# Optimization experiments

Measured on AMD Instinct MI355X. Metric: run time of the kernel, lower is better.

Reference implementation:

```python
import jax, jax.numpy as jnp
import numpy as np

B, SQ, SK, D, H, DFF = 4, 1024, 1024, 1024, 16, 4096
DEPTH = D // H
EPS = 1e-6


def setup_inputs() -> dict:
    key = jax.random.key(0)
    ks = jax.random.split(key, 32)
    s = 0.02
    inp = {
        "x": jax.random.normal(ks[0], (B, SQ, D), jnp.float32),
        "enc_output": jax.random.normal(ks[1], (B, SK, D), jnp.float32),
        # causal look-ahead mask: 1 where attention is disallowed
        "look_ahead_mask": (1.0 - jnp.tril(jnp.ones((SQ, SQ), jnp.float32)))[None, None],
        "padding_mask": jnp.zeros((B, 1, 1, SK), jnp.float32),
    }
    names = ["wq1", "wk1", "wv1", "wo1", "wq2", "wk2", "wv2", "wo2"]
    for i, n in enumerate(names):
        inp[n] = jax.random.normal(ks[2 + i], (D, D), jnp.float32) * s
        inp["b" + n[1:]] = jnp.zeros((D,), jnp.float32)
    inp["w_ffn1"] = jax.random.normal(ks[12], (D, DFF), jnp.float32) * s
    inp["b_ffn1"] = jnp.zeros((DFF,), jnp.float32)
    inp["w_ffn2"] = jax.random.normal(ks[13], (DFF, D), jnp.float32) * s
    inp["b_ffn2"] = jnp.zeros((D,), jnp.float32)
    for i in (1, 2, 3):
        inp[f"gamma{i}"] = jnp.ones((D,), jnp.float32)
        inp[f"beta{i}"] = jnp.zeros((D,), jnp.float32)
    return inp


def _layernorm(x, gamma, beta):
    mu = jnp.mean(x, axis=-1, keepdims=True)
    var = jnp.var(x, axis=-1, keepdims=True)
    return (x - mu) * jax.lax.rsqrt(var + EPS) * gamma + beta


def _split_heads(x):
    b, s, _ = x.shape
    return x.reshape(b, s, H, DEPTH).transpose(0, 2, 1, 3)  # (B,H,S,depth)


def _mha(v_in, k_in, q_in, mask, wq, bq, wk, bk, wv, bv, wo, bo):
    q = _split_heads(q_in @ wq + bq)
    k = _split_heads(k_in @ wk + bk)
    v = _split_heads(v_in @ wv + bv)
    logits = jnp.einsum("bhqd,bhkd->bhqk", q, k) / jnp.sqrt(jnp.float32(DEPTH))
    if mask is not None:
        logits = logits + mask * -1e9
    attn = jax.nn.softmax(logits, axis=-1)
    out = jnp.einsum("bhqk,bhkd->bhqd", attn, v)
    out = out.transpose(0, 2, 1, 3).reshape(q_in.shape[0], -1, D)
    return out @ wo + bo, attn


def reference(x, enc_output, look_ahead_mask, padding_mask,
              wq1, bq1, wk1, bk1, wv1, bv1, wo1, bo1,
              wq2, bq2, wk2, bk2, wv2, bv2, wo2, bo2,
              w_ffn1, b_ffn1, w_ffn2, b_ffn2,
              gamma1, beta1, gamma2, beta2, gamma3, beta3):
    attn1, aw1 = _mha(x, x, x, look_ahead_mask,
                      wq1, bq1, wk1, bk1, wv1, bv1, wo1, bo1)
    out1 = _layernorm(attn1 + x, gamma1, beta1)
    attn2, aw2 = _mha(enc_output, enc_output, out1, padding_mask,
                      wq2, bq2, wk2, bk2, wv2, bv2, wo2, bo2)
    out2 = _layernorm(attn2 + out1, gamma2, beta2)
    ffn = jax.nn.relu(out2 @ w_ffn1 + b_ffn1) @ w_ffn2 + b_ffn2
    out3 = _layernorm(ffn + out2, gamma3, beta3)
    return out3, aw1, aw2
```

## Files before the change

kernel.cpp:

```cpp
#include <hip/hip_runtime.h>

#define NB 4
#define SEQ 1024
#define DM 1024
#define NH 16
#define DEP 64
#define DFFN 4096

typedef __attribute__((ext_vector_type(8))) short short8;
typedef __attribute__((ext_vector_type(4))) float f32x4;
typedef __attribute__((ext_vector_type(4))) unsigned short us4;

__device__ __forceinline__ unsigned short f2bf(float f) {
    union { float f; unsigned int u; } v; v.f = f;
    unsigned int u = v.u;
    return (unsigned short)((u + 0x7FFFu + ((u >> 16) & 1u)) >> 16);
}

__device__ __forceinline__ void gload16(const void* g, void* l) {
    __builtin_amdgcn_global_load_lds((const __attribute__((address_space(1))) unsigned int*)g,
                                     (__attribute__((address_space(3))) unsigned int*)l, 16, 0, 0);
}

__global__ __launch_bounds__(256) void cast2_kernel(const float* __restrict__ a,
                                                    const float* __restrict__ b,
                                                    unsigned short* __restrict__ oa,
                                                    unsigned short* __restrict__ ob, int n4) {
    int i = blockIdx.x * 256 + threadIdx.x;
    const float* in = blockIdx.y ? b : a;
    unsigned short* out = blockIdx.y ? ob : oa;
    if (i < n4) {
        float4 f = ((const float4*)in)[i];
        us4 u;
        u[0] = f2bf(f.x); u[1] = f2bf(f.y); u[2] = f2bf(f.z); u[3] = f2bf(f.w);
        ((us4*)out)[i] = u;
    }
}

struct P10 { const float* p[10]; };
__global__ __launch_bounds__(256) void castTall_kernel(P10 s,
                                                       unsigned short* __restrict__ wsq,
                                                       unsigned short* __restrict__ wf1t,
                                                       unsigned short* __restrict__ wf2t) {
    __shared__ float tile[64][65];
    const int tid = blockIdx.x, t = threadIdx.x;
    const float* in; unsigned short* out; int R, C, r0, c0;
    if (tid < 2048) {
        int wi = tid >> 8, t2 = tid & 255;
        in = s.p[wi]; out = wsq + (size_t)wi * DM * DM; R = DM; C = DM;
        r0 = (t2 >> 4) * 64; c0 = (t2 & 15) * 64;
    } else if (tid < 3072) {
        int t2 = tid - 2048;
        in = s.p[8]; out = wf1t; R = DM; C = DFFN;
        r0 = (t2 >> 6) * 64; c0 = (t2 & 63) * 64;
    } else {
        int t2 = tid - 3072;
        in = s.p[9]; out = wf2t; R = DFFN; C = DM;
        r0 = (t2 >> 4) * 64; c0 = (t2 & 15) * 64;
    }
#pragma unroll
    for (int p = 0; p < 4; ++p) {
        int r = p * 16 + (t >> 4), c = (t & 15) * 4;
        float4 f = *(const float4*)(in + (size_t)(r0 + r) * C + c0 + c);
        tile[r][c] = f.x; tile[r][c + 1] = f.y; tile[r][c + 2] = f.z; tile[r][c + 3] = f.w;
    }
    __syncthreads();
#pragma unroll
    for (int p = 0; p < 4; ++p) {
        int n = p * 16 + (t >> 4), k = (t & 15) * 4;
        us4 u;
#pragma unroll
        for (int j = 0; j < 4; ++j) u[j] = f2bf(tile[k + j][n]);
        *(us4*)(out + (size_t)(c0 + n) * R + r0 + k) = u;
    }
}

__global__ __launch_bounds__(256) void biaspack_kernel(const float* __restrict__ bq1,
                                                       const float* __restrict__ bk1,
                                                       const float* __restrict__ bv1,
                                                       const float* __restrict__ bk2,
                                                       const float* __restrict__ bv2,
                                                       float* __restrict__ bqkv1,
                                                       float* __restrict__ bkv2) {
    int i = blockIdx.x * 256 + threadIdx.x;
    if (i < 1024) bqkv1[i] = bq1[i];
    else if (i < 2048) bqkv1[i] = bk1[i - 1024];
    else if (i < 3072) bqkv1[i] = bv1[i - 2048];
    else if (i < 4096) bkv2[i - 3072] = bk2[i - 3072];
    else if (i < 5120) bkv2[i - 3072] = bv2[i - 4096];
}

template <int BM, int BN, int BK, int KSPLIT, int RELU, int WB, int WF, int WVT>
__global__ __launch_bounds__(256) void gemm_kernel(const unsigned short* __restrict__ A,
                                                   const unsigned short* __restrict__ Wt,
                                                   const float* __restrict__ bias,
                                                   unsigned short* __restrict__ Cb,
                                                   float* __restrict__ Cf,
                                                   float* __restrict__ Cf2,
                                                   unsigned short* __restrict__ Vt,
                                                   int vstart,
                                                   int M, int N, int K) {
    constexpr int AM = BM / 32;
    constexpr int KS = BK / 32;
    constexpr int LPR = BK / 8;
    constexpr int RPI = 64 / LPR;
    constexpr int AR = (BM / 4) / RPI;
    constexpr int BR = (BN / 4) / RPI;
    __shared__ unsigned short As[BM * BK];
    __shared__ unsigned short Bs[BN * BK];
    const int t = threadIdx.x;
    const int lane = t & 63, w = t >> 6;
    const int m0 = blockIdx.y * BM, n0 = blockIdx.x * BN;
    const int wm = (w >> 1) * (BM / 2), wn = (w & 1) * (BN / 2);
    const int lr = lane & 15, g = lane >> 4, kb = g * 8;
    const int srow = lane / LPR, scol = (lane % LPR) * 8;
    const int kofs = (KSPLIT == 2 && blockIdx.z) ? K / 2 : 0;
    const int Keff = (KSPLIT == 2) ? K / 2 : K;

    f32x4 acc[AM][4];
#pragma unroll
    for (int a = 0; a < AM; ++a)
#pragma unroll
        for (int b = 0; b < 4; ++b)
#pragma unroll
            for (int j = 0; j < 4; ++j) acc[a][b][j] = 0.f;

    for (int kt = 0; kt < Keff; kt += BK) {
        __syncthreads();
#pragma unroll
        for (int ia = 0; ia < AR; ++ia) {
            int rb = w * (BM / 4) + ia * RPI;
            gload16(A + (size_t)(m0 + rb + srow) * K + kofs + kt + scol, As + rb * BK);
        }
#pragma unroll
        for (int ib = 0; ib < BR; ++ib) {
            int rb = w * (BN / 4) + ib * RPI;
            gload16(Wt + (size_t)(n0 + rb + srow) * K + kofs + kt + scol, Bs + rb * BK);
        }
        __syncthreads();

        short8 af[AM][KS], bfr[4][KS];
#pragma unroll
        for (int i = 0; i < AM; ++i)
#pragma unroll
            for (int ks = 0; ks < KS; ++ks)
                af[i][ks] = *(const short8*)&As[(wm + i * 16 + lr) * BK + ks * 32 + kb];
#pragma unroll
        for (int i = 0; i < 4; ++i)
#pragma unroll
            for (int ks = 0; ks < KS; ++ks)
                bfr[i][ks] = *(const short8*)&Bs[(wn + i * 16 + lr) * BK + ks * 32 + kb];
#pragma unroll
        for (int ks = 0; ks < KS; ++ks)
#pragma unroll
            for (int am = 0; am < AM; ++am)
#pragma unroll
                for (int bn = 0; bn < 4; ++bn)
                    acc[am][bn] = __builtin_amdgcn_mfma_f32_16x16x32_bf16(af[am][ks], bfr[bn][ks], acc[am][bn], 0, 0, 0);
    }

    float* cfo = (KSPLIT == 2 && blockIdx.z) ? Cf2 : Cf;
    const bool addb = bias && (KSPLIT == 1 || blockIdx.z == 0);
#pragma unroll
    for (int am = 0; am < AM; ++am) {
#pragma unroll
        for (int bn = 0; bn < 4; ++bn) {
            int col = n0 + wn + bn * 16 + lr;
            float bv = addb ? bias[col] : 0.f;
            int rowb = m0 + wm + am * 16 + g * 4;
            float vv[4];
#pragma unroll
            for (int i = 0; i < 4; ++i) {
                float v = acc[am][bn][i] + bv;
                if (RELU) v = v > 0.f ? v : 0.f;
                vv[i] = v;
                if (WF) cfo[(size_t)(rowb + i) * N + col] = v;
                if (WB) Cb[(size_t)(rowb + i) * N + col] = f2bf(v);
            }
            if (WVT && col >= vstart) {
                int h = (col - vstart) >> 6, dep = (col - vstart) & 63;
                int b = rowb >> 10, kpos = rowb & 1023;
                us4 u;
#pragma unroll
                for (int i = 0; i < 4; ++i) u[i] = f2bf(vv[i]);
                *(us4*)(Vt + ((size_t)(b * NH + h) * DEP + dep) * SEQ + kpos) = u;
            }
        }
    }
}

template <int CAUSAL>
__global__ __launch_bounds__(256, 2) void attn_kernel(const unsigned short* __restrict__ Q, int ldq,
                                                      const unsigned short* __restrict__ Kp, int ldk,
                                                      const unsigned short* __restrict__ Vt,
                                                      const float* __restrict__ pad,
                                                      float* __restrict__ aw,
                                                      unsigned short* __restrict__ ctx) {
    __shared__ unsigned short Ks[2][128 * 64];
    __shared__ unsigned short Pch[32 * 128];
    __shared__ float redm[4][32];
    __shared__ float reds[4][32];
    const int t = threadIdx.x, lane = t & 63, w = t >> 6;
    const int lr = lane & 15, g = lane >> 4;
    const int id = blockIdx.x;
    const int bh = (id & 7) + ((id >> 8) << 3);
    const int qt = (id >> 3) & 31;
    const int q0 = qt * 32;
    const int b = bh >> 4, h = bh & 15;
    const size_t qbase = (size_t)b * SEQ * ldq + (size_t)h * DEP;
    const size_t kbase = (size_t)b * SEQ * ldk + (size_t)h * DEP;
    const int cmax = CAUSAL ? (q0 >> 7) + 1 : 8;

    const int srow = lane >> 3;
    const int sslot = (lane & 7) ^ srow;

    short8 aq[2][2];
#pragma unroll
    for (int p = 0; p < 2; ++p)
#pragma unroll
        for (int ks = 0; ks < 2; ++ks)
            aq[p][ks] = *(const short8*)(Q + qbase + (size_t)(q0 + p * 16 + lr) * ldq + ks * 32 + g * 8);

    f32x4 acc[2][8][2];
#pragma unroll
    for (int p = 0; p < 2; ++p)
#pragma unroll
        for (int c = 0; c < 8; ++c)
#pragma unroll
            for (int bn = 0; bn < 2; ++bn)
#pragma unroll
                for (int j = 0; j < 4; ++j) acc[p][c][bn][j] = 0.f;

    {
#pragma unroll
        for (int i = 0; i < 4; ++i) {
            int rb = w * 32 + i * 8;
            gload16(Kp + kbase + (size_t)(rb + srow) * ldk + sslot * 8, &Ks[0][rb * 64]);
        }
    }
#pragma unroll
    for (int c = 0; c < 8; ++c) {
        if (c < cmax) {
            __syncthreads();
            if (c + 1 < cmax) {
#pragma unroll
                for (int i = 0; i < 4; ++i) {
                    int rb = w * 32 + i * 8;
                    gload16(Kp + kbase + (size_t)((c + 1) * 128 + rb + srow) * ldk + sslot * 8,
                            &Ks[(c + 1) & 1][rb * 64]);
                }
            }
#pragma unroll
            for (int ks = 0; ks < 2; ++ks)
#pragma unroll
                for (int bn = 0; bn < 2; ++bn) {
                    int row = w * 32 + bn * 16 + lr;
                    short8 bk = *(const short8*)((const char*)&Ks[c & 1][0] + row * 128 +
                                                 ((ks * 64 + g * 16) ^ ((lr & 7) << 4)));
                    acc[0][c][bn] = __builtin_amdgcn_mfma_f32_16x16x32_bf16(bk, aq[0][ks], acc[0][c][bn], 0, 0, 0);
                    acc[1][c][bn] = __builtin_amdgcn_mfma_f32_16x16x32_bf16(bk, aq[1][ks], acc[1][c][bn], 0, 0, 0);
                }
        }
    }

    float mrow[2] = {-1e30f, -1e30f};
#pragma unroll
    for (int c = 0; c < 8; ++c) {
        if (c < cmax) {
#pragma unroll
            for (int bn = 0; bn < 2; ++bn) {
                int k4 = c * 128 + w * 32 + bn * 16 + g * 4;
                f32x4 pv = {0.f, 0.f, 0.f, 0.f};
                if (pad) pv = *(const f32x4*)(pad + (size_t)b * SEQ + k4);
#pragma unroll
                for (int p = 0; p < 2; ++p) {
                    int q = q0 + p * 16 + lr;
#pragma unroll
                    for (int i = 0; i < 4; ++i) {
                        float v = acc[p][c][bn][i] * 0.125f + pv[i] * -1e9f;
                        if (CAUSAL && (k4 + i) > q) v = -1e30f;
                        acc[p][c][bn][i] = v;
                        mrow[p] = fmaxf(mrow[p], v);
                    }
                }
            }
        }
    }
#pragma unroll
    for (int p = 0; p < 2; ++p) {
        mrow[p] = fmaxf(mrow[p], __shfl_xor(mrow[p], 16));
        mrow[p] = fmaxf(mrow[p], __shfl_xor(mrow[p], 32));
    }
    if (lane < 16) { redm[w][lr] = mrow[0]; redm[w][16 + lr] = mrow[1]; }
    __syncthreads();
    float Mv[2];
#pragma unroll
    for (int p = 0; p < 2; ++p)
        Mv[p] = fmaxf(fmaxf(redm[0][p * 16 + lr], redm[1][p * 16 + lr]),
                      fmaxf(redm[2][p * 16 + lr], redm[3][p * 16 + lr]));

    float srw[2] = {0.f, 0.f};
#pragma unroll
    for (int c = 0; c < 8; ++c) {
        if (c < cmax) {
#pragma unroll
            for (int p = 0; p < 2; ++p)
#pragma unroll
                for (int bn = 0; bn < 2; ++bn)
#pragma unroll
                    for (int i = 0; i < 4; ++i) {
                        float e = __expf(acc[p][c][bn][i] - Mv[p]);
                        acc[p][c][bn][i] = e;
                        srw[p] += e;
                    }
        }
    }
#pragma unroll
    for (int p = 0; p < 2; ++p) {
        srw[p] += __shfl_xor(srw[p], 16);
        srw[p] += __shfl_xor(srw[p], 32);
    }
    if (lane < 16) { reds[w][lr] = srw[0]; reds[w][16 + lr] = srw[1]; }
    __syncthreads();
    float inv[2];
#pragma unroll
    for (int p = 0; p < 2; ++p)
        inv[p] = 1.0f / (reds[0][p * 16 + lr] + reds[1][p * 16 + lr] +
                         reds[2][p * 16 + lr] + reds[3][p * 16 + lr]);

    f32x4 acc2[2];
#pragma unroll
    for (int p = 0; p < 2; ++p)
#pragma unroll
        for (int j = 0; j < 4; ++j) acc2[p][j] = 0.f;
    char* pch = (char*)Pch;
    const int sw = (lr & 7) << 4;
#pragma unroll
    for (int c = 0; c < 8; ++c) {
        if (c < cmax) {
            __syncthreads();
#pragma unroll
            for (int p = 0; p < 2; ++p)
#pragma unroll
                for (int bn = 0; bn < 2; ++bn) {
                    us4 u;
#pragma unroll
                    for (int i = 0; i < 4; ++i) u[i] = f2bf(acc[p][c][bn][i] * inv[p]);
                    *(us4*)(pch + (p * 16 + lr) * 256 + ((w * 64 + bn * 32 + g * 8) ^ sw)) = u;
                }
            __syncthreads();
#pragma unroll
            for (int ks = 0; ks < 4; ++ks) {
                short8 bf = *(const short8*)(Vt + ((size_t)bh * DEP + w * 16 + lr) * SEQ + c * 128 + ks * 32 + g * 8);
#pragma unroll
                for (int p = 0; p < 2; ++p) {
                    short8 af = *(const short8*)(pch + (p * 16 + lr) * 256 + ((ks * 64 + g * 16) ^ sw));
                    acc2[p] = __builtin_amdgcn_mfma_f32_16x16x32_bf16(af, bf, acc2[p], 0, 0, 0);
                }
            }
        }
    }
#pragma unroll
    for (int p = 0; p < 2; ++p)
#pragma unroll
        for (int i = 0; i < 4; ++i)
            ctx[((size_t)b * SEQ + q0 + p * 16 + g * 4 + i) * DM + h * DEP + w * 16 + lr] = f2bf(acc2[p][i]);

#pragma unroll
    for (int p = 0; p < 2; ++p) {
        float* awrow = aw + ((size_t)bh * SEQ + q0 + p * 16 + lr) * SEQ;
#pragma unroll
        for (int c = 0; c < 8; ++c)
#pragma unroll
            for (int bn = 0; bn < 2; ++bn) {
                f32x4 o = {0.f, 0.f, 0.f, 0.f};
                if (c < cmax) {
#pragma unroll
                    for (int i = 0; i < 4; ++i) o[i] = acc[p][c][bn][i] * inv[p];
                }
                *(f32x4*)(awrow + c * 128 + w * 32 + bn * 16 + g * 4) = o;
            }
    }
}

template <int WB, int X2EN>
__global__ __launch_bounds__(256) void ln_kernel(const float* __restrict__ X,
                                                 const float* __restrict__ X2,
                                                 const float* __restrict__ R,
                                                 const float* __restrict__ gamma,
                                                 const float* __restrict__ beta,
                                                 float* __restrict__ outF,
                                                 unsigned short* __restrict__ outB) {
    size_t row = blockIdx.x;
    const int t = threadIdx.x;
    float4 a = ((const float4*)(X + (row << 10)))[t];
    float4 r = ((const float4*)(R + (row << 10)))[t];
    float v0 = a.x + r.x, v1 = a.y + r.y, v2 = a.z + r.z, v3 = a.w + r.w;
    if (X2EN) {
        float4 a2 = ((const float4*)(X2 + (row << 10)))[t];
        v0 += a2.x; v1 += a2.y; v2 += a2.z; v3 += a2.w;
    }
    float s = v0 + v1 + v2 + v3;
    float q = v0 * v0 + v1 * v1 + v2 * v2 + v3 * v3;
#pragma unroll
    for (int off = 32; off; off >>= 1) {
        s += __shfl_down(s, off);
        q += __shfl_down(q, off);
    }
    __shared__ float rs[4], rq[4];
    if ((t & 63) == 0) { rs[t >> 6] = s; rq[t >> 6] = q; }
    __syncthreads();
    s = rs[0] + rs[1] + rs[2] + rs[3];
    q = rq[0] + rq[1] + rq[2] + rq[3];
    float mean = s * (1.0f / 1024.0f);
    float var = q * (1.0f / 1024.0f) - mean * mean;
    float inv = rsqrtf(var + 1e-6f);
    float g0 = gamma[t * 4], g1 = gamma[t * 4 + 1], g2 = gamma[t * 4 + 2], g3 = gamma[t * 4 + 3];
    float b0 = beta[t * 4], b1 = beta[t * 4 + 1], b2 = beta[t * 4 + 2], b3 = beta[t * 4 + 3];
    float o0 = (v0 - mean) * inv * g0 + b0;
    float o1 = (v1 - mean) * inv * g1 + b1;
    float o2 = (v2 - mean) * inv * g2 + b2;
    float o3 = (v3 - mean) * inv * g3 + b3;
    float4 o; o.x = o0; o.y = o1; o.z = o2; o.w = o3;
    ((float4*)(outF + (row << 10)))[t] = o;
    if (WB) {
        us4 u;
        u[0] = f2bf(o0); u[1] = f2bf(o1); u[2] = f2bf(o2); u[3] = f2bf(o3);
        ((us4*)(outB + (row << 10)))[t] = u;
    }
}

extern "C" void kernel_launch(void* const* d_in, const int* in_sizes, int n_in,
                              void* d_out, int out_size, void* d_ws, size_t ws_size,
                              hipStream_t stream) {
    const float* x = (const float*)d_in[0];
    const float* enc = (const float*)d_in[1];
    const float* pad = (const float*)d_in[3];
    const float* wq1 = (const float*)d_in[4];  const float* bq1 = (const float*)d_in[5];
    const float* wk1 = (const float*)d_in[6];  const float* bk1 = (const float*)d_in[7];
    const float* wv1 = (const float*)d_in[8];  const float* bv1 = (const float*)d_in[9];
    const float* wo1 = (const float*)d_in[10]; const float* bo1 = (const float*)d_in[11];
    const float* wq2 = (const float*)d_in[12]; const float* bq2 = (const float*)d_in[13];
    const float* wk2 = (const float*)d_in[14]; const float* bk2 = (const float*)d_in[15];
    const float* wv2 = (const float*)d_in[16]; const float* bv2 = (const float*)d_in[17];
    const float* wo2 = (const float*)d_in[18]; const float* bo2 = (const float*)d_in[19];
    const float* wf1 = (const float*)d_in[20]; const float* bf1 = (const float*)d_in[21];
    const float* wf2 = (const float*)d_in[22]; const float* bf2 = (const float*)d_in[23];
    const float* g1 = (const float*)d_in[24]; const float* be1 = (const float*)d_in[25];
    const float* g2 = (const float*)d_in[26]; const float* be2 = (const float*)d_in[27];
    const float* g3 = (const float*)d_in[28]; const float* be3 = (const float*)d_in[29];

    float* out3 = (float*)d_out;
    float* aw1 = out3 + (size_t)NB * SEQ * DM;
    float* aw2 = aw1 + (size_t)NB * NH * SEQ * SEQ;

    char* ws = (char*)d_ws;
    size_t off = 0;
    auto take = [&](size_t n) { char* p = ws + off; off += (n + 255) & ~(size_t)255; return p; };
    const size_t SZ_SD_BF = (size_t)NB * SEQ * DM * 2;
    const size_t SZ_SD_F  = (size_t)NB * SEQ * DM * 4;
    const size_t SZ_DD_BF = (size_t)DM * DM * 2;

    unsigned short* wqkv1t = (unsigned short*)take(3 * SZ_DD_BF);
    unsigned short* wq2t   = (unsigned short*)take(SZ_DD_BF);
    unsigned short* wkv2t  = (unsigned short*)take(2 * SZ_DD_BF);
    unsigned short* wo1t   = (unsigned short*)take(SZ_DD_BF);
    unsigned short* wo2t   = (unsigned short*)take(SZ_DD_BF);
    unsigned short* wf1t   = (unsigned short*)take((size_t)DM * DFFN * 2);
    unsigned short* wf2t   = (unsigned short*)take((size_t)DFFN * DM * 2);
    float* bqkv1 = (float*)take(3 * DM * 4);
    float* bkv2  = (float*)take(2 * DM * 4);
    unsigned short* xb    = (unsigned short*)take(SZ_SD_BF);
    unsigned short* encb  = (unsigned short*)take(SZ_SD_BF);
    unsigned short* qkv1b = (unsigned short*)take(3 * SZ_SD_BF);
    unsigned short* v1t   = (unsigned short*)take(SZ_SD_BF);
    unsigned short* qb    = (unsigned short*)take(SZ_SD_BF);
    unsigned short* kv2b  = (unsigned short*)take(2 * SZ_SD_BF);
    unsigned short* v2t   = (unsigned short*)take(SZ_SD_BF);
    unsigned short* ctx   = (unsigned short*)take(SZ_SD_BF);
    float* goutf  = (float*)take(SZ_SD_F);
    float* gout2f = (float*)take(SZ_SD_F);
    float* out1f  = (float*)take(SZ_SD_F);
    unsigned short* out1b = (unsigned short*)take(SZ_SD_BF);
    float* out2f  = (float*)take(SZ_SD_F);
    unsigned short* out2b = (unsigned short*)take(SZ_SD_BF);
    unsigned short* ffn1b = (unsigned short*)take((size_t)NB * SEQ * DFFN * 2);

    {
        int n4 = NB * SEQ * DM / 4;
        dim3 gc((n4 + 255) / 256, 2);
        cast2_kernel<<<gc, 256, 0, stream>>>(x, enc, xb, encb, n4);
    }
    {
        P10 s;
        s.p[0] = wq1; s.p[1] = wk1; s.p[2] = wv1; s.p[3] = wq2;
        s.p[4] = wk2; s.p[5] = wv2; s.p[6] = wo1; s.p[7] = wo2;
        s.p[8] = wf1; s.p[9] = wf2;
        castTall_kernel<<<4096, 256, 0, stream>>>(s, wqkv1t, wf1t, wf2t);
    }
    biaspack_kernel<<<20, 256, 0, stream>>>(bq1, bk1, bv1, bk2, bv2, bqkv1, bkv2);

    const int M = NB * SEQ;
    dim3 gQKV(3 * DM / 128, M / 128);
    dim3 gKV(2 * DM / 128, M / 128);
    dim3 gDD64(DM / 128, M / 64);
    dim3 gDF(DFFN / 128, M / 128);
    dim3 gF2(DM / 128, M / 128, 2);

    gemm_kernel<128, 128, 32, 1, 0, 1, 0, 1><<<gQKV, 256, 0, stream>>>(xb, wqkv1t, bqkv1, qkv1b, nullptr, nullptr, v1t, 2048, M, 3 * DM, DM);
    attn_kernel<1><<<2048, 256, 0, stream>>>(qkv1b, 3 * DM, qkv1b + DM, 3 * DM, v1t, nullptr, aw1, ctx);
    gemm_kernel<64, 128, 64, 1, 0, 0, 1, 0><<<gDD64, 256, 0, stream>>>(ctx, wo1t, bo1, nullptr, goutf, nullptr, nullptr, 0, M, DM, DM);
    ln_kernel<1, 0><<<M, 256, 0, stream>>>(goutf, nullptr, x, g1, be1, out1f, out1b);

    gemm_kernel<64, 128, 64, 1, 0, 1, 0, 0><<<gDD64, 256, 0, stream>>>(out1b, wq2t, bq2, qb, nullptr, nullptr, nullptr, 0, M, DM, DM);
    gemm_kernel<128, 128, 32, 1, 0, 1, 0, 1><<<gKV, 256, 0, stream>>>(encb, wkv2t, bkv2, kv2b, nullptr, nullptr, v2t, 1024, M, 2 * DM, DM);
    attn_kernel<0><<<2048, 256, 0, stream>>>(qb, DM, kv2b, 2 * DM, v2t, pad, aw2, ctx);
    gemm_kernel<64, 128, 64, 1, 0, 0, 1, 0><<<gDD64, 256, 0, stream>>>(ctx, wo2t, bo2, nullptr, goutf, nullptr, nullptr, 0, M, DM, DM);
    ln_kernel<1, 0><<<M, 256, 0, stream>>>(goutf, nullptr, out1f, g2, be2, out2f, out2b);

    gemm_kernel<128, 128, 32, 1, 1, 1, 0, 0><<<gDF, 256, 0, stream>>>(out2b, wf1t, bf1, ffn1b, nullptr, nullptr, nullptr, 0, M, DFFN, DM);
    gemm_kernel<128, 128, 32, 2, 0, 0, 1, 0><<<gF2, 256, 0, stream>>>(ffn1b, wf2t, bf2, nullptr, goutf, gout2f, nullptr, 0, M, DM, DFFN);
    ln_kernel<0, 1><<<M, 256, 0, stream>>>(goutf, gout2f, out2f, g3, be3, out3, nullptr);
}
```

Baseline: 577.7 us.

## Double-buffer GEMM LDS staging, swizzle tile order, add nontemporal loads/stores

The GEMM kernel now double-buffers its A/B LDS tiles. It issues the next K-slice's global-to-LDS loads before computing the current one and uses vmcnt waits plus raw barriers instead of two __syncthreads per iteration. Block IDs are remapped with an 8-way swizzle so that consecutive workgroups share operand tiles in L2. Separately, the weight and input cast kernels use nontemporal loads, and the attention-weight output and the final layernorm output use nontemporal stores to avoid polluting the cache. Double buffering doubles the GEMM's LDS footprint, which may lower occupancy.

```diff
diff --git a/kernel.cpp b/kernel.cpp
--- a/kernel.cpp
+++ b/kernel.cpp
@@ -30,9 +30,9 @@
     const float* in = blockIdx.y ? b : a;
     unsigned short* out = blockIdx.y ? ob : oa;
     if (i < n4) {
-        float4 f = ((const float4*)in)[i];
+        f32x4 f = __builtin_nontemporal_load((const f32x4*)in + i);
         us4 u;
-        u[0] = f2bf(f.x); u[1] = f2bf(f.y); u[2] = f2bf(f.z); u[3] = f2bf(f.w);
+        u[0] = f2bf(f[0]); u[1] = f2bf(f[1]); u[2] = f2bf(f[2]); u[3] = f2bf(f[3]);
         ((us4*)out)[i] = u;
     }
 }
@@ -61,8 +61,8 @@
 #pragma unroll
     for (int p = 0; p < 4; ++p) {
         int r = p * 16 + (t >> 4), c = (t & 15) * 4;
-        float4 f = *(const float4*)(in + (size_t)(r0 + r) * C + c0 + c);
-        tile[r][c] = f.x; tile[r][c + 1] = f.y; tile[r][c + 2] = f.z; tile[r][c + 3] = f.w;
+        f32x4 f = __builtin_nontemporal_load((const f32x4*)(in + (size_t)(r0 + r) * C + c0 + c));
+        tile[r][c] = f[0]; tile[r][c + 1] = f[1]; tile[r][c + 2] = f[2]; tile[r][c + 3] = f[3];
     }
     __syncthreads();
 #pragma unroll
@@ -106,16 +106,21 @@
     constexpr int RPI = 64 / LPR;
     constexpr int AR = (BM / 4) / RPI;
     constexpr int BR = (BN / 4) / RPI;
-    __shared__ unsigned short As[BM * BK];
-    __shared__ unsigned short Bs[BN * BK];
+    constexpr int NLD = AR + BR;
+    __shared__ unsigned short As[2][BM * BK];
+    __shared__ unsigned short Bs[2][BN * BK];
     const int t = threadIdx.x;
     const int lane = t & 63, w = t >> 6;
-    const int m0 = blockIdx.y * BM, n0 = blockIdx.x * BN;
+    const int nwg = gridDim.x * gridDim.y;
+    const int rawid = blockIdx.y * gridDim.x + blockIdx.x;
+    const int swz = (rawid & 7) * (nwg >> 3) + (rawid >> 3);
+    const int m0 = (swz / gridDim.x) * BM, n0 = (swz % gridDim.x) * BN;
     const int wm = (w >> 1) * (BM / 2), wn = (w & 1) * (BN / 2);
     const int lr = lane & 15, g = lane >> 4, kb = g * 8;
     const int srow = lane / LPR, scol = (lane % LPR) * 8;
     const int kofs = (KSPLIT == 2 && blockIdx.z) ? K / 2 : 0;
     const int Keff = (KSPLIT == 2) ? K / 2 : K;
+    const int nk = Keff / BK;
 
     f32x4 acc[AM][4];
 #pragma unroll
@@ -125,31 +130,41 @@
 #pragma unroll
             for (int j = 0; j < 4; ++j) acc[a][b][j] = 0.f;
 
-    for (int kt = 0; kt < Keff; kt += BK) {
-        __syncthreads();
+    auto STAGE = [&](int buf, int kt) {
 #pragma unroll
         for (int ia = 0; ia < AR; ++ia) {
             int rb = w * (BM / 4) + ia * RPI;
-            gload16(A + (size_t)(m0 + rb + srow) * K + kofs + kt + scol, As + rb * BK);
+            gload16(A + (size_t)(m0 + rb + srow) * K + kt + scol, &As[buf][rb * BK]);
         }
 #pragma unroll
         for (int ib = 0; ib < BR; ++ib) {
             int rb = w * (BN / 4) + ib * RPI;
-            gload16(Wt + (size_t)(n0 + rb + srow) * K + kofs + kt + scol, Bs + rb * BK);
-        }
-        __syncthreads();
+            gload16(Wt + (size_t)(n0 + rb + srow) * K + kt + scol, &Bs[buf][rb * BK]);
+        }
+    };
+
+    STAGE(0, kofs);
+    for (int i = 0; i < nk; ++i) {
+        const int cur = i & 1;
+        if (i + 1 < nk) {
+            STAGE(cur ^ 1, kofs + (i + 1) * BK);
+            asm volatile("s_waitcnt vmcnt(%0)" :: "n"(NLD) : "memory");
+        } else {
+            asm volatile("s_waitcnt vmcnt(0)" ::: "memory");
+        }
+        __builtin_amdgcn_s_barrier();
 
         short8 af[AM][KS], bfr[4][KS];
 #pragma unroll
-        for (int i = 0; i < AM; ++i)
+        for (int ii = 0; ii < AM; ++ii)
 #pragma unroll
             for (int ks = 0; ks < KS; ++ks)
-                af[i][ks] = *(const short8*)&As[(wm + i * 16 + lr) * BK + ks * 32 + kb];
-#pragma unroll
-        for (int i = 0; i < 4; ++i)
+                af[ii][ks] = *(const short8*)&As[cur][(wm + ii * 16 + lr) * BK + ks * 32 + kb];
+#pragma unroll
+        for (int ii = 0; ii < 4; ++ii)
 #pragma unroll
             for (int ks = 0; ks < KS; ++ks)
-                bfr[i][ks] = *(const short8*)&Bs[(wn + i * 16 + lr) * BK + ks * 32 + kb];
+                bfr[ii][ks] = *(const short8*)&Bs[cur][(wn + ii * 16 + lr) * BK + ks * 32 + kb];
 #pragma unroll
         for (int ks = 0; ks < KS; ++ks)
 #pragma unroll
@@ -157,6 +172,7 @@
 #pragma unroll
                 for (int bn = 0; bn < 4; ++bn)
                     acc[am][bn] = __builtin_amdgcn_mfma_f32_16x16x32_bf16(af[am][ks], bfr[bn][ks], acc[am][bn], 0, 0, 0);
+        __builtin_amdgcn_s_barrier();
     }
 
     float* cfo = (KSPLIT == 2 && blockIdx.z) ? Cf2 : Cf;
@@ -378,12 +394,12 @@
 #pragma unroll
                     for (int i = 0; i < 4; ++i) o[i] = acc[p][c][bn][i] * inv[p];
                 }
-                *(f32x4*)(awrow + c * 128 + w * 32 + bn * 16 + g * 4) = o;
+                __builtin_nontemporal_store(o, (f32x4*)(awrow + c * 128 + w * 32 + bn * 16 + g * 4));
             }
     }
 }
 
-template <int WB, int X2EN>
+template <int WB, int X2EN, int NTF>
 __global__ __launch_bounds__(256) void ln_kernel(const float* __restrict__ X,
                                                  const float* __restrict__ X2,
                                                  const float* __restrict__ R,
@@ -417,15 +433,16 @@
     float inv = rsqrtf(var + 1e-6f);
     float g0 = gamma[t * 4], g1 = gamma[t * 4 + 1], g2 = gamma[t * 4 + 2], g3 = gamma[t * 4 + 3];
     float b0 = beta[t * 4], b1 = beta[t * 4 + 1], b2 = beta[t * 4 + 2], b3 = beta[t * 4 + 3];
-    float o0 = (v0 - mean) * inv * g0 + b0;
-    float o1 = (v1 - mean) * inv * g1 + b1;
-    float o2 = (v2 - mean) * inv * g2 + b2;
-    float o3 = (v3 - mean) * inv * g3 + b3;
-    float4 o; o.x = o0; o.y = o1; o.z = o2; o.w = o3;
-    ((float4*)(outF + (row << 10)))[t] = o;
+    f32x4 o;
+    o[0] = (v0 - mean) * inv * g0 + b0;
+    o[1] = (v1 - mean) * inv * g1 + b1;
+    o[2] = (v2 - mean) * inv * g2 + b2;
+    o[3] = (v3 - mean) * inv * g3 + b3;
+    if (NTF) __builtin_nontemporal_store(o, (f32x4*)(outF + (row << 10)) + t);
+    else ((f32x4*)(outF + (row << 10)))[t] = o;
     if (WB) {
         us4 u;
-        u[0] = f2bf(o0); u[1] = f2bf(o1); u[2] = f2bf(o2); u[3] = f2bf(o3);
+        u[0] = f2bf(o[0]); u[1] = f2bf(o[1]); u[2] = f2bf(o[2]); u[3] = f2bf(o[3]);
         ((us4*)(outB + (row << 10)))[t] = u;
     }
 }
@@ -510,15 +527,15 @@
     gemm_kernel<128, 128, 32, 1, 0, 1, 0, 1><<<gQKV, 256, 0, stream>>>(xb, wqkv1t, bqkv1, qkv1b, nullptr, nullptr, v1t, 2048, M, 3 * DM, DM);
     attn_kernel<1><<<2048, 256, 0, stream>>>(qkv1b, 3 * DM, qkv1b + DM, 3 * DM, v1t, nullptr, aw1, ctx);
     gemm_kernel<64, 128, 64, 1, 0, 0, 1, 0><<<gDD64, 256, 0, stream>>>(ctx, wo1t, bo1, nullptr, goutf, nullptr, nullptr, 0, M, DM, DM);
-    ln_kernel<1, 0><<<M, 256, 0, stream>>>(goutf, nullptr, x, g1, be1, out1f, out1b);
+    ln_kernel<1, 0, 0><<<M, 256, 0, stream>>>(goutf, nullptr, x, g1, be1, out1f, out1b);
 
     gemm_kernel<64, 128, 64, 1, 0, 1, 0, 0><<<gDD64, 256, 0, stream>>>(out1b, wq2t, bq2, qb, nullptr, nullptr, nullptr, 0, M, DM, DM);
     gemm_kernel<128, 128, 32, 1, 0, 1, 0, 1><<<gKV, 256, 0, stream>>>(encb, wkv2t, bkv2, kv2b, nullptr, nullptr, v2t, 1024, M, 2 * DM, DM);
     attn_kernel<0><<<2048, 256, 0, stream>>>(qb, DM, kv2b, 2 * DM, v2t, pad, aw2, ctx);
     gemm_kernel<64, 128, 64, 1, 0, 0, 1, 0><<<gDD64, 256, 0, stream>>>(ctx, wo2t, bo2, nullptr, goutf, nullptr, nullptr, 0, M, DM, DM);
-    ln_kernel<1, 0><<<M, 256, 0, stream>>>(goutf, nullptr, out1f, g2, be2, out2f, out2b);
+    ln_kernel<1, 0, 0><<<M, 256, 0, stream>>>(goutf, nullptr, out1f, g2, be2, out2f, out2b);
 
     gemm_kernel<128, 128, 32, 1, 1, 1, 0, 0><<<gDF, 256, 0, stream>>>(out2b, wf1t, bf1, ffn1b, nullptr, nullptr, nullptr, 0, M, DFFN, DM);
     gemm_kernel<128, 128, 32, 2, 0, 0, 1, 0><<<gF2, 256, 0, stream>>>(ffn1b, wf2t, bf2, nullptr, goutf, gout2f, nullptr, 0, M, DM, DFFN);
-    ln_kernel<0, 1><<<M, 256, 0, stream>>>(goutf, gout2f, out2f, g3, be3, out3, nullptr);
-}
+    ln_kernel<0, 1, 1><<<M, 256, 0, stream>>>(goutf, gout2f, out2f, g3, be3, out3, nullptr);
+}
```

After: 505.2 us. 1.14x faster.
